# Optimization experiments

Measured on AMD Instinct MI355X. Metric: run time of the kernel, lower is better.

## Reference

```python
import jax, jax.numpy as jnp
import numpy as np
from jax import lax

B, L, E = 16, 100, 128
NQ, NC, DL = 1000, 100, 100
NODE, PATH, MAXC = 5000, 5000, 128


def setup_inputs() -> dict:
    key = jax.random.key(0)
    ks = jax.random.split(key, 40)
    rn = lambda k, *s: jax.random.normal(k, s, jnp.float32) * 0.02
    inp = {}
    inp['code'] = jax.random.randint(ks[0], (B, L, NQ * 2 + MAXC * 3), 0, NODE, jnp.int32)
    inp['q'] = jax.random.randint(ks[1], (B, L), 0, NQ, jnp.int32)
    inp['c'] = jax.random.randint(ks[2], (B, L), 0, NC, jnp.int32)
    inp['sd'] = jax.random.randint(ks[3], (B, L), 0, DL, jnp.int32)
    inp['qd'] = jax.random.randint(ks[4], (B, L), 0, DL, jnp.int32)
    inp['a'] = jax.random.randint(ks[5], (B, L), 0, NQ * 2, jnp.int32)
    inp['qshft'] = jax.random.randint(ks[6], (B, L), 0, NQ, jnp.int32)
    inp['cshft'] = jax.random.randint(ks[7], (B, L), 0, NC, jnp.int32)
    inp['sdshft'] = jax.random.randint(ks[8], (B, L), 0, DL, jnp.int32)
    inp['qdshft'] = jax.random.randint(ks[9], (B, L), 0, DL, jnp.int32)
    # embedding tables (padding rows zeroed, matching torch padding_idx)
    inp['embed_nodes'] = rn(ks[10], NODE + 2, E)
    inp['embed_paths'] = rn(ks[11], PATH + 2, E)
    inp['q_tab'] = rn(ks[12], NQ + 1, E).at[NQ].set(0.0)
    inp['c_tab'] = rn(ks[13], NC + 1, E).at[NC].set(0.0)
    inp['sd_tab'] = rn(ks[14], DL + 100, E).at[0].set(0.0)
    inp['qd_tab'] = rn(ks[15], DL + 100, E).at[0].set(0.0)
    inp['a_tab'] = rn(ks[16], NQ * 2 + 2, E).at[2].set(0.0)
    inp['knowledge'] = rn(ks[17], 1, E)
    # linear weights stored [in, out] so y = x @ W + b
    inp['Wpt'] = rn(ks[18], 3 * E, 3 * E); inp['bpt'] = rn(ks[19], 3 * E)
    inp['Wat'] = rn(ks[20], 3 * E, 1);     inp['bat'] = rn(ks[21], 1)
    inp['Wqa'] = rn(ks[22], 4 * E, E);     inp['bqa'] = rn(ks[23], E)
    inp['W1'] = rn(ks[24], 4 * E, E);      inp['b1'] = rn(ks[25], E)
    inp['W2'] = rn(ks[26], E, E);          inp['b2'] = rn(ks[27], E)
    inp['W3'] = rn(ks[28], E, E);          inp['b3'] = rn(ks[29], E)
    inp['W4'] = rn(ks[30], 2 * E, E);      inp['b4'] = rn(ks[31], E)
    inp['W5'] = rn(ks[32], 2 * E, E);      inp['b5'] = rn(ks[33], E)
    inp['W6'] = rn(ks[34], 4 * E, E);      inp['b6'] = rn(ks[35], E)
    inp['Wf'] = rn(ks[36], E, 10);         inp['bf'] = rn(ks[37], 10)
    return inp


def reference(code, q, c, sd, qd, a, qshft, cshft, sdshft, qdshft,
              embed_nodes, embed_paths, q_tab, c_tab, sd_tab, qd_tab, a_tab,
              knowledge, Wpt, bpt, Wat, bat, Wqa, bqa, W1, b1, W2, b2, W3, b3,
              W4, b4, W5, b5, W6, b6, Wf, bf):
    Bq, Lq = q.shape
    # ---- code2vec attention over AST paths ----
    c2v = code[:, :, NQ * 2:].reshape(Bq, Lq, MAXC, 3)
    full = jnp.concatenate([embed_nodes[c2v[..., 0]],
                            embed_nodes[c2v[..., 2]],
                            embed_paths[c2v[..., 1]]], axis=-1)  # [B,L,MAXC,3E]
    tr = jnp.tanh(full @ Wpt + bpt)
    ctx = tr @ Wat + bat                      # [B,L,MAXC,1]
    attn = jax.nn.softmax(ctx, axis=1)        # softmax over seq dim (dim=1), as in source
    code_vec = jnp.sum(full * attn, axis=2)   # [B,L,3E]
    # ---- embeddings + input projections ----
    a_e = a_tab[a]
    acode = jnp.concatenate([a_e, code_vec], axis=-1) @ Wqa + bqa   # [B,L,E]
    inp = jnp.concatenate([q_tab[q], c_tab[c], sd_tab[sd], qd_tab[qd]], axis=-1) @ W1 + b1
    sd_e = sd_tab[sd]
    qd_e = qd_tab[qd]
    # ---- sequential SDF/PKA/KSU recurrence ----
    k0 = jnp.tile(knowledge, (Bq, 1))  # [B,E]

    def step(k, ts):
        inp_t, a_t, sd_t, qd_t = ts
        qq = inp_t - k
        sdf = jax.nn.sigmoid(qq @ W2 + b2) * jnp.tanh(qq @ W3 + b3)
        x = jnp.concatenate([sdf, a_t], axis=-1)
        pka = jax.nn.sigmoid(x @ W4 + b4) * jnp.tanh(x @ W5 + b5)
        ins = jnp.concatenate([k, a_t, sd_t, qd_t], axis=-1)
        g = jax.nn.sigmoid(ins @ W6 + b6)
        k_new = g * k + (1.0 - g) * pka
        return k_new, k_new @ Wf + bf

    xs = (inp.transpose(1, 0, 2), acode.transpose(1, 0, 2),
          sd_e.transpose(1, 0, 2), qd_e.transpose(1, 0, 2))
    _, logits = lax.scan(step, k0, xs)        # [L,B,10]
    return jax.nn.sigmoid(logits.transpose(1, 0, 2))  # [B,L,10]
```

## Files before the change

### kernel.cpp

```cpp
#include <hip/hip_runtime.h>
#include <hip/hip_bf16.h>

#define B_   16
#define L_   100
#define E_   128
#define NQ_  1000
#define MAXC_ 128
#define CODE_STRIDE (NQ_*2 + MAXC_*3)
#define CODE_OFF    (NQ_*2)

typedef short bf16x8 __attribute__((ext_vector_type(8)));
typedef float f32x4  __attribute__((ext_vector_type(4)));

__device__ __forceinline__ unsigned short f2b(float f) {
    unsigned u = __float_as_uint(f);
    unsigned r = (u + 0x7fffu + ((u >> 16) & 1u)) >> 16;
    return (unsigned short)r;
}
__device__ __forceinline__ unsigned cvt2(float lo, float hi) {
    unsigned r;
    asm("v_cvt_pk_bf16_f32 %0, %1, %2" : "=v"(r) : "v"(lo), "v"(hi));
    return r;
}
__device__ __forceinline__ float fsig(float x) {
    return __builtin_amdgcn_rcpf(1.0f + __builtin_amdgcn_exp2f(-1.44269504f * x));
}
__device__ __forceinline__ float ftanh(float x) {
    return 1.0f - 2.0f * __builtin_amdgcn_rcpf(1.0f + __builtin_amdgcn_exp2f(2.88539008f * x));
}
__device__ __forceinline__ void ldsbar() {
    asm volatile("s_waitcnt lgkmcnt(0)" ::: "memory");
    __builtin_amdgcn_s_barrier();
}
__device__ __forceinline__ void vmbar() {
    asm volatile("s_waitcnt vmcnt(0) lgkmcnt(0)" ::: "memory");
    __builtin_amdgcn_s_barrier();
}
__device__ __forceinline__ void gll16(const void* g, void* l) {
    __builtin_amdgcn_global_load_lds(
        (const __attribute__((address_space(1))) unsigned int*)g,
        (__attribute__((address_space(3))) unsigned int*)l, 16, 0, 0);
}

__global__ void k_prep(const float* __restrict__ Wpt, const float* __restrict__ en,
                       const float* __restrict__ ep,
                       const float* __restrict__ W2, const float* __restrict__ W3,
                       const float* __restrict__ W4, const float* __restrict__ W5,
                       const float* __restrict__ W6, const float* __restrict__ Wf,
                       const float* __restrict__ Wqa, const float* __restrict__ W1,
                       unsigned short* __restrict__ wptT, unsigned short* __restrict__ enb,
                       unsigned short* __restrict__ epb, unsigned short* __restrict__ bt1,
                       unsigned short* __restrict__ bt2, unsigned short* __restrict__ btf,
                       unsigned short* __restrict__ bW1, unsigned short* __restrict__ bW2,
                       unsigned short* __restrict__ bW6)
{
    int i = blockIdx.x * 256 + threadIdx.x;
    switch (blockIdx.y) {
    case 0: if (i < 384*384) {
                int e = i & 7, G = i >> 3;
                int l15g = G & 15, rest = G >> 4;
                int l4g = rest & 3, rest2 = rest >> 2;
                int ksg = rest2 % 12, tile = rest2 / 12;
                int n = tile*16 + l15g, k = ksg*32 + l4g*8 + e;
                wptT[i] = f2b(Wpt[k*384 + n]);
            } break;
    case 1: if (i < 5002*128) enb[i] = f2b(en[i]); break;
    case 2: if (i < 5002*128) epb[i] = f2b(ep[i]); break;
    case 3: if (i < 384*128) {
                int n = i >> 7, k = i & 127;
                float v = (n < 128) ? W2[k*128 + n] : (n < 256) ? W3[k*128 + (n-128)]
                                                                : W6[k*128 + (n-256)];
                bt1[i] = f2b(v);
            } break;
    case 4: if (i < 256*128) {
                int n = i >> 7, k = i & 127;
                float v = (n < 128) ? W4[k*128 + n] : W5[k*128 + (n-128)];
                bt2[i] = f2b(v);
            } break;
    case 5: if (i < 16*128) {
                int n = i >> 7, k = i & 127;
                btf[i] = f2b(n < 10 ? Wf[k*10 + n] : 0.0f);
            } break;
    case 6: if (i < 256*512) {
                int n = i >> 9, k = i & 511;
                float v = (n < 128) ? Wqa[k*128 + n] : W1[k*128 + (n-128)];
                bW1[i] = f2b(v);
            } break;
    case 7: if (i < 512*128) {
                int n = i >> 7, k = i & 127;
                float v = (n < 128) ? W2[k*128 + n]
                        : (n < 256) ? W3[k*128 + (n-128)]
                        : (n < 384) ? W4[(128 + k)*128 + (n-256)]
                                    : W5[(128 + k)*128 + (n-384)];
                bW2[i] = f2b(v);
            } break;
    case 8: if (i < 128*384) {
                int n = i / 384, k = i % 384;
                bW6[i] = f2b(W6[(128 + k)*128 + n]);
            } break;
    }
}

__global__ __launch_bounds__(256, 3) void k_ctx(const int* __restrict__ code,
    const unsigned short* __restrict__ enb, const unsigned short* __restrict__ epb,
    const unsigned short* __restrict__ wptT, const float* __restrict__ bpt,
    const float* __restrict__ wat, const float* __restrict__ bat,
    float* __restrict__ ctx)
{
    __shared__ __align__(16) unsigned short Bs[2][12288];
    __shared__ float bw[768];
    const int tid = threadIdx.x, wv = tid >> 6, lane = tid & 63;
    const int l15 = lane & 15, l4 = lane >> 4;
    const int rowg0 = blockIdx.x * 128;

    for (int idx = tid; idx < 768; idx += 256)
        bw[idx] = (idx < 384) ? bpt[idx] : wat[idx - 384];

    bf16x8 af[2][12];
    #pragma unroll
    for (int h = 0; h < 2; ++h) {
        int rowg = rowg0 + h * 64 + wv * 16 + l15;
        int m = rowg & 127, bl = rowg >> 7;
        const int* cp = code + (size_t)bl * CODE_STRIDE + CODE_OFF + m * 3;
        int i0 = cp[0], i1 = cp[1], i2 = cp[2];
        #pragma unroll
        for (int ks = 0; ks < 12; ++ks) {
            int seg = ks >> 2;
            int idx = (seg == 0) ? i0 : (seg == 1 ? i2 : i1);
            const unsigned short* tab = (seg == 2) ? epb : enb;
            af[h][ks] = *(const bf16x8*)(tab + (size_t)idx * 128 + (ks & 3) * 32 + l4 * 8);
        }
    }

    {
        const unsigned short* src = wptT;
        #pragma unroll
        for (int i = 0; i < 6; ++i) {
            int jj = wv * 6 + i;
            gll16(src + jj * 512 + lane * 8, &Bs[0][jj * 512]);
        }
    }

    float cr[2][4] = {{0.f,0.f,0.f,0.f},{0.f,0.f,0.f,0.f}};
    const float bat0 = bat[0];

    for (int nc = 0; nc < 12; ++nc) {
        vmbar();
        if (nc < 11) {
            const unsigned short* src = wptT + (size_t)(nc + 1) * 12288;
            #pragma unroll
            for (int i = 0; i < 6; ++i) {
                int jj = wv * 6 + i;
                gll16(src + jj * 512 + lane * 8, &Bs[(nc + 1) & 1][jj * 512]);
            }
        }
        const char* bb0 = (const char*)&Bs[nc & 1][0] + l15 * 16;
        const char* bb1 = bb0 + 12288;
        f32x4 acc00 = {0.f,0.f,0.f,0.f}, acc01 = {0.f,0.f,0.f,0.f};
        f32x4 acc10 = {0.f,0.f,0.f,0.f}, acc11 = {0.f,0.f,0.f,0.f};
        #pragma unroll
        for (int ks = 0; ks < 12; ++ks) {
            int go = (ks * 4 + l4) * 256;
            bf16x8 b0 = *(const bf16x8*)(bb0 + go);
            bf16x8 b1 = *(const bf16x8*)(bb1 + go);
            acc00 = __builtin_amdgcn_mfma_f32_16x16x32_bf16(af[0][ks], b0, acc00, 0, 0, 0);
            acc01 = __builtin_amdgcn_mfma_f32_16x16x32_bf16(af[0][ks], b1, acc01, 0, 0, 0);
            acc10 = __builtin_amdgcn_mfma_f32_16x16x32_bf16(af[1][ks], b0, acc10, 0, 0, 0);
            acc11 = __builtin_amdgcn_mfma_f32_16x16x32_bf16(af[1][ks], b1, acc11, 0, 0, 0);
        }
        int ng0 = nc * 32 + l15, ng1 = ng0 + 16;
        float bv0 = bw[ng0], wa0 = bw[384 + ng0];
        float bv1 = bw[ng1], wa1 = bw[384 + ng1];
        #pragma unroll
        for (int r = 0; r < 4; ++r) {
            cr[0][r] += ftanh(acc00[r] + bv0) * wa0 + ftanh(acc01[r] + bv1) * wa1;
            cr[1][r] += ftanh(acc10[r] + bv0) * wa0 + ftanh(acc11[r] + bv1) * wa1;
        }
    }

    #pragma unroll
    for (int h = 0; h < 2; ++h)
        #pragma unroll
        for (int r = 0; r < 4; ++r) {
            float v = cr[h][r];
            v += __shfl_xor(v, 1); v += __shfl_xor(v, 2);
            v += __shfl_xor(v, 4); v += __shfl_xor(v, 8);
            cr[h][r] = v;
        }
    if (l15 == 0) {
        #pragma unroll
        for (int h = 0; h < 2; ++h) {
            int rbase = rowg0 + h * 64 + wv * 16 + l4 * 4;
            #pragma unroll
            for (int r = 0; r < 4; ++r) ctx[rbase + r] = cr[h][r] + bat0;
        }
    }
}

__global__ void k_softmax(const float* __restrict__ ctx, float* __restrict__ attn)
{
    int t = blockIdx.x * 256 + threadIdx.x;
    if (t >= B_ * MAXC_) return;
    int b = t >> 7, m = t & 127;
    const float* p = ctx + (size_t)b * L_ * MAXC_ + m;
    float mx = -1e30f;
    for (int l = 0; l < L_; ++l) mx = fmaxf(mx, p[l * MAXC_]);
    float s = 0.f;
    for (int l = 0; l < L_; ++l) s += __expf(p[l * MAXC_] - mx);
    float inv = 1.0f / s;
    float* o = attn + (size_t)b * L_ * MAXC_ + m;
    for (int l = 0; l < L_; ++l) o[l * MAXC_] = __expf(p[l * MAXC_] - mx) * inv;
}

__global__ __launch_bounds__(192) void k_codevec(const int* __restrict__ code,
    const float* __restrict__ attn, const unsigned short* __restrict__ enb,
    const unsigned short* __restrict__ epb, float* __restrict__ cv)
{
    int bl = blockIdx.x;
    int t = threadIdx.x;
    int seg = t >> 6, tc = t & 63;
    const int* cp = code + (size_t)bl * CODE_STRIDE + CODE_OFF;
    const float* ap = attn + (size_t)bl * MAXC_;
    const unsigned short* tab = (seg == 2) ? epb : enb;
    const int sidx = (seg == 0) ? 0 : (seg == 1) ? 2 : 1;
    float ax = 0.f, ay = 0.f;
    #pragma unroll 8
    for (int m = 0; m < MAXC_; ++m) {
        float w = ap[m];
        int idx = cp[m * 3 + sidx];
        unsigned u = *((const unsigned*)(tab + (size_t)idx * 128) + tc);
        ax += w * __uint_as_float(u << 16);
        ay += w * __uint_as_float(u & 0xffff0000u);
    }
    float2 o; o.x = ax; o.y = ay;
    *(float2*)(cv + (size_t)bl * 384 + seg * 128 + tc * 2) = o;
}

__global__ __launch_bounds__(256) void k_fuse(
    const int* __restrict__ a, const int* __restrict__ q, const int* __restrict__ c,
    const int* __restrict__ sd, const int* __restrict__ qd,
    const float* __restrict__ a_tab, const float* __restrict__ q_tab,
    const float* __restrict__ c_tab, const float* __restrict__ sd_tab,
    const float* __restrict__ qd_tab, const float* __restrict__ cv,
    const unsigned short* __restrict__ bW1, const unsigned short* __restrict__ bW2,
    const unsigned short* __restrict__ bW6,
    const float* __restrict__ bqa, const float* __restrict__ b1,
    const float* __restrict__ b2, const float* __restrict__ b3,
    const float* __restrict__ b4, const float* __restrict__ b5,
    const float* __restrict__ b6,
    float4* __restrict__ preQ, float* __restrict__ pre6)
{
    __shared__ __align__(16) unsigned short X[16 * 1024];
    __shared__ __align__(16) unsigned short Y[16 * 256];
    const int tid = threadIdx.x, wv = tid >> 6, lane = tid & 63;
    const int l15 = lane & 15, l4 = lane >> 4;
    const int row0 = blockIdx.x * 16;

    #pragma unroll
    for (int it = 0; it < 16; ++it) {
        int idx = tid + it * 256;
        int r = idx >> 8, col = (idx & 255) * 4;
        int row = row0 + r;
        const float* src;
        if (col < 128)       src = a_tab + (size_t)a[row] * 128 + col;
        else if (col < 512)  src = cv + (size_t)row * 384 + (col - 128);
        else if (col < 640)  src = q_tab + (size_t)q[row] * 128 + (col - 512);
        else if (col < 768)  src = c_tab + (size_t)c[row] * 128 + (col - 640);
        else if (col < 896)  src = sd_tab + (size_t)sd[row] * 128 + (col - 768);
        else                 src = qd_tab + (size_t)qd[row] * 128 + (col - 896);
        float4 v = *(const float4*)src;
        unsigned u0 = cvt2(v.x, v.y), u1 = cvt2(v.z, v.w);
        int byte = r * 2048 + ((((col >> 3)) ^ (r & 7)) << 4) + ((col & 4) << 1);
        *(unsigned*)((char*)X + byte) = u0;
        *(unsigned*)((char*)X + byte + 4) = u1;
    }
    ldsbar();

    {
        bf16x8 ak[16];
        int kbase = (wv < 2) ? 0 : 512;
        #pragma unroll
        for (int ks = 0; ks < 16; ++ks) {
            int col = kbase + ks * 32 + l4 * 8;
            ak[ks] = *(const bf16x8*)((const char*)X + l15 * 2048 + (((col >> 3) ^ (l15 & 7)) << 4));
        }
        int nbase = wv * 64;
        f32x4 acc[4] = {{0,0,0,0},{0,0,0,0},{0,0,0,0},{0,0,0,0}};
        #pragma unroll
        for (int i = 0; i < 4; ++i) {
            const unsigned short* bp = bW1 + (size_t)(nbase + i * 16 + l15) * 512 + l4 * 8;
            #pragma unroll
            for (int ks = 0; ks < 16; ++ks) {
                bf16x8 bfr = *(const bf16x8*)(bp + ks * 32);
                acc[i] = __builtin_amdgcn_mfma_f32_16x16x32_bf16(ak[ks], bfr, acc[i], 0, 0, 0);
            }
        }
        #pragma unroll
        for (int i = 0; i < 4; ++i) {
            int cc = nbase + i * 16 + l15;
            float bias = (cc < 128) ? bqa[cc] : b1[cc - 128];
            #pragma unroll
            for (int rr = 0; rr < 4; ++rr) {
                int row = l4 * 4 + rr;
                int byte = row * 512 + (((cc >> 3) ^ (row & 7)) << 4) + (cc & 7) * 2;
                *(unsigned short*)((char*)Y + byte) = f2b(acc[i][rr] + bias);
            }
        }
    }
    ldsbar();

    bf16x8 zi[4], za[4], zs[4], zq[4];
    #pragma unroll
    for (int ks = 0; ks < 4; ++ks) {
        int ci = 128 + ks * 32 + l4 * 8;
        zi[ks] = *(const bf16x8*)((const char*)Y + l15 * 512 + (((ci >> 3) ^ (l15 & 7)) << 4));
        int ca = ks * 32 + l4 * 8;
        za[ks] = *(const bf16x8*)((const char*)Y + l15 * 512 + (((ca >> 3) ^ (l15 & 7)) << 4));
        int cs = 768 + ks * 32 + l4 * 8;
        zs[ks] = *(const bf16x8*)((const char*)X + l15 * 2048 + (((cs >> 3) ^ (l15 & 7)) << 4));
        int cq = 896 + ks * 32 + l4 * 8;
        zq[ks] = *(const bf16x8*)((const char*)X + l15 * 2048 + (((cq >> 3) ^ (l15 & 7)) << 4));
    }
    f32x4 A2[2] = {{0,0,0,0},{0,0,0,0}}, A3[2] = {{0,0,0,0},{0,0,0,0}};
    f32x4 A4[2] = {{0,0,0,0},{0,0,0,0}}, A5[2] = {{0,0,0,0},{0,0,0,0}};
    f32x4 A6[2] = {{0,0,0,0},{0,0,0,0}};
    #pragma unroll
    for (int tt = 0; tt < 2; ++tt) {
        int n = wv * 32 + tt * 16 + l15;
        const unsigned short* p2 = bW2 + (size_t)(      n) * 128 + l4 * 8;
        const unsigned short* p3 = bW2 + (size_t)(128 + n) * 128 + l4 * 8;
        const unsigned short* p4 = bW2 + (size_t)(256 + n) * 128 + l4 * 8;
        const unsigned short* p5 = bW2 + (size_t)(384 + n) * 128 + l4 * 8;
        const unsigned short* p6 = bW6 + (size_t)n * 384 + l4 * 8;
        #pragma unroll
        for (int ks = 0; ks < 4; ++ks) {
            A2[tt] = __builtin_amdgcn_mfma_f32_16x16x32_bf16(zi[ks], *(const bf16x8*)(p2 + ks*32), A2[tt], 0, 0, 0);
            A3[tt] = __builtin_amdgcn_mfma_f32_16x16x32_bf16(zi[ks], *(const bf16x8*)(p3 + ks*32), A3[tt], 0, 0, 0);
            A4[tt] = __builtin_amdgcn_mfma_f32_16x16x32_bf16(za[ks], *(const bf16x8*)(p4 + ks*32), A4[tt], 0, 0, 0);
            A5[tt] = __builtin_amdgcn_mfma_f32_16x16x32_bf16(za[ks], *(const bf16x8*)(p5 + ks*32), A5[tt], 0, 0, 0);
            A6[tt] = __builtin_amdgcn_mfma_f32_16x16x32_bf16(za[ks], *(const bf16x8*)(p6 + ks*32), A6[tt], 0, 0, 0);
        }
        #pragma unroll
        for (int ks = 0; ks < 4; ++ks)
            A6[tt] = __builtin_amdgcn_mfma_f32_16x16x32_bf16(zs[ks], *(const bf16x8*)(p6 + 256 + ks*32), A6[tt], 0, 0, 0);
        #pragma unroll
        for (int ks = 0; ks < 4; ++ks)
            A6[tt] = __builtin_amdgcn_mfma_f32_16x16x32_bf16(zq[ks], *(const bf16x8*)(p6 + 512 + ks*32), A6[tt], 0, 0, 0);
    }
    #pragma unroll
    for (int tt = 0; tt < 2; ++tt) {
        int n = wv * 32 + tt * 16 + l15;
        float c2 = b2[n], c3 = b3[n], c4 = b4[n], c5 = b5[n], c6 = b6[n];
        #pragma unroll
        for (int rr = 0; rr < 4; ++rr) {
            size_t row = (size_t)(row0 + l4 * 4 + rr);
            float4 o;
            o.x = A2[tt][rr] + c2; o.y = A3[tt][rr] + c3;
            o.z = A4[tt][rr] + c4; o.w = A5[tt][rr] + c5;
            preQ[row * 128 + n] = o;
            pre6[row * 128 + n] = A6[tt][rr] + c6;
        }
    }
}

__global__ __launch_bounds__(512) void k_recur(
    const unsigned short* __restrict__ bt1, const unsigned short* __restrict__ bt2,
    const float* __restrict__ knowledge, const float4* __restrict__ preQ,
    const float* __restrict__ pre6, unsigned short* __restrict__ khist)
{
    __shared__ __align__(16) unsigned short k_lds[16 * 128];
    __shared__ __align__(16) unsigned short s_lds[16 * 128];
    const int tid = threadIdx.x, wv = tid >> 6, lane = tid & 63;
    const int l15 = lane & 15, l4 = lane >> 4;
    const int j = wv * 16 + l15;

    bf16x8 w2f[4], w3f[4], w6f[4], w4f[4], w5f[4];
    #pragma unroll
    for (int ks = 0; ks < 4; ++ks) {
        w2f[ks] = *(const bf16x8*)(bt1 + (size_t)(      j) * 128 + ks * 32 + l4 * 8);
        w3f[ks] = *(const bf16x8*)(bt1 + (size_t)(128 + j) * 128 + ks * 32 + l4 * 8);
        w6f[ks] = *(const bf16x8*)(bt1 + (size_t)(256 + j) * 128 + ks * 32 + l4 * 8);
        w4f[ks] = *(const bf16x8*)(bt2 + (size_t)(      j) * 128 + ks * 32 + l4 * 8);
        w5f[ks] = *(const bf16x8*)(bt2 + (size_t)(128 + j) * 128 + ks * 32 + l4 * 8);
    }

    float kreg[4], gR[4];
    {
        float k0 = knowledge[j];
        unsigned short kb = f2b(k0);
        #pragma unroll
        for (int r = 0; r < 4; ++r) {
            kreg[r] = k0;
            int b = l4 * 4 + r;
            k_lds[b * 128 + (((j >> 3) ^ b) << 3) + (j & 7)] = kb;
        }
    }
    ldsbar();

    float4 pv[4]; float p6[4];
    #pragma unroll
    for (int r = 0; r < 4; ++r) {
        int b = l4 * 4 + r;
        size_t ix = (size_t)(b * L_) * 128 + j;
        pv[r] = preQ[ix]; p6[r] = pre6[ix];
    }

    for (int t = 0; t < L_; ++t) {
        float4 pvN[4]; float p6N[4];
        #pragma unroll
        for (int r = 0; r < 4; ++r) {
            int b = l4 * 4 + r;
            size_t ix = (size_t)(b * L_ + t + 1) * 128 + j;
            pvN[r] = preQ[ix]; p6N[r] = pre6[ix];
        }

        bf16x8 ak[4];
        {
            const unsigned short* kb = k_lds + l15 * 128;
            #pragma unroll
            for (int ks = 0; ks < 4; ++ks)
                ak[ks] = *(const bf16x8*)(kb + (((ks * 4 + l4) ^ l15) << 3));
        }
        f32x4 a2 = {0,0,0,0}, a3 = {0,0,0,0}, a6 = {0,0,0,0};
        #pragma unroll
        for (int ks = 0; ks < 4; ++ks) {
            a2 = __builtin_amdgcn_mfma_f32_16x16x32_bf16(ak[ks], w2f[ks], a2, 0, 0, 0);
            a3 = __builtin_amdgcn_mfma_f32_16x16x32_bf16(ak[ks], w3f[ks], a3, 0, 0, 0);
            a6 = __builtin_amdgcn_mfma_f32_16x16x32_bf16(ak[ks], w6f[ks], a6, 0, 0, 0);
        }
        #pragma unroll
        for (int r = 0; r < 4; ++r) {
            int b = l4 * 4 + r;
            float sdf = fsig(pv[r].x - a2[r]) * ftanh(pv[r].y - a3[r]);
            gR[r] = fsig(a6[r] + p6[r]);
            s_lds[b * 128 + (((j >> 3) ^ b) << 3) + (j & 7)] = f2b(sdf);
        }
        ldsbar();
        bf16x8 as[4];
        {
            const unsigned short* sb = s_lds + l15 * 128;
            #pragma unroll
            for (int ks = 0; ks < 4; ++ks)
                as[ks] = *(const bf16x8*)(sb + (((ks * 4 + l4) ^ l15) << 3));
        }
        f32x4 a4 = {0,0,0,0}, a5 = {0,0,0,0};
        #pragma unroll
        for (int ks = 0; ks < 4; ++ks) {
            a4 = __builtin_amdgcn_mfma_f32_16x16x32_bf16(as[ks], w4f[ks], a4, 0, 0, 0);
            a5 = __builtin_amdgcn_mfma_f32_16x16x32_bf16(as[ks], w5f[ks], a5, 0, 0, 0);
        }
        #pragma unroll
        for (int r = 0; r < 4; ++r) {
            int b = l4 * 4 + r;
            float pka = fsig(a4[r] + pv[r].z) * ftanh(a5[r] + pv[r].w);
            float kn = gR[r] * kreg[r] + (1.0f - gR[r]) * pka;
            kreg[r] = kn;
            unsigned short kb2 = f2b(kn);
            k_lds[b * 128 + (((j >> 3) ^ b) << 3) + (j & 7)] = kb2;
            khist[(size_t)(b * L_ + t) * 128 + j] = kb2;
        }
        #pragma unroll
        for (int r = 0; r < 4; ++r) { pv[r] = pvN[r]; p6[r] = p6N[r]; }
        ldsbar();
    }
}

__global__ __launch_bounds__(256) void k_logits(const unsigned short* __restrict__ khist,
    const unsigned short* __restrict__ btf, const float* __restrict__ bfv,
    float* __restrict__ out)
{
    int wv = threadIdx.x >> 6, lane = threadIdx.x & 63;
    int l15 = lane & 15, l4 = lane >> 4;
    int R0 = (blockIdx.x * 4 + wv) * 16;
    bf16x8 wbf[4], akr[4];
    #pragma unroll
    for (int ks = 0; ks < 4; ++ks)
        wbf[ks] = *(const bf16x8*)(btf + (size_t)l15 * 128 + ks * 32 + l4 * 8);
    const unsigned short* kb = khist + (size_t)(R0 + l15) * 128;
    #pragma unroll
    for (int ks = 0; ks < 4; ++ks)
        akr[ks] = *(const bf16x8*)(kb + ks * 32 + l4 * 8);
    f32x4 af = {0.f, 0.f, 0.f, 0.f};
    #pragma unroll
    for (int ks = 0; ks < 4; ++ks)
        af = __builtin_amdgcn_mfma_f32_16x16x32_bf16(akr[ks], wbf[ks], af, 0, 0, 0);
    if (l15 < 10) {
        float bb = bfv[l15];
        #pragma unroll
        for (int r = 0; r < 4; ++r)
            out[(size_t)(R0 + l4 * 4 + r) * 10 + l15] = fsig(af[r] + bb);
    }
}

extern "C" void kernel_launch(void* const* d_in, const int* in_sizes, int n_in,
                              void* d_out, int out_size, void* d_ws, size_t ws_size,
                              hipStream_t stream)
{
    const int*   code  = (const int*)d_in[0];
    const int*   q     = (const int*)d_in[1];
    const int*   c     = (const int*)d_in[2];
    const int*   sd    = (const int*)d_in[3];
    const int*   qd    = (const int*)d_in[4];
    const int*   a     = (const int*)d_in[5];
    const float* en    = (const float*)d_in[10];
    const float* ep    = (const float*)d_in[11];
    const float* q_tab = (const float*)d_in[12];
    const float* c_tab = (const float*)d_in[13];
    const float* sd_tab= (const float*)d_in[14];
    const float* qd_tab= (const float*)d_in[15];
    const float* a_tab = (const float*)d_in[16];
    const float* know  = (const float*)d_in[17];
    const float* Wpt   = (const float*)d_in[18];
    const float* bpt   = (const float*)d_in[19];
    const float* Wat   = (const float*)d_in[20];
    const float* bat   = (const float*)d_in[21];
    const float* Wqa   = (const float*)d_in[22];
    const float* bqa   = (const float*)d_in[23];
    const float* W1    = (const float*)d_in[24];
    const float* b1    = (const float*)d_in[25];
    const float* W2    = (const float*)d_in[26];
    const float* b2    = (const float*)d_in[27];
    const float* W3    = (const float*)d_in[28];
    const float* b3    = (const float*)d_in[29];
    const float* W4    = (const float*)d_in[30];
    const float* b4    = (const float*)d_in[31];
    const float* W5    = (const float*)d_in[32];
    const float* b5    = (const float*)d_in[33];
    const float* W6    = (const float*)d_in[34];
    const float* b6    = (const float*)d_in[35];
    const float* Wf    = (const float*)d_in[36];
    const float* bf_   = (const float*)d_in[37];

    char* ws = (char*)d_ws;
    size_t off = 0;
    auto alloc = [&](size_t n) { size_t r = off; off += (n + 255) & ~(size_t)255; return r; };
    unsigned short* wptT = (unsigned short*)(ws + alloc(384 * 384 * 2));
    unsigned short* enb  = (unsigned short*)(ws + alloc(5002 * 128 * 2));
    unsigned short* epb  = (unsigned short*)(ws + alloc(5002 * 128 * 2));
    unsigned short* bt1  = (unsigned short*)(ws + alloc(384 * 128 * 2));
    unsigned short* bt2  = (unsigned short*)(ws + alloc(256 * 128 * 2));
    unsigned short* btf  = (unsigned short*)(ws + alloc(16 * 128 * 2));
    unsigned short* bW1  = (unsigned short*)(ws + alloc(256 * 512 * 2));
    unsigned short* bW2  = (unsigned short*)(ws + alloc(512 * 128 * 2));
    unsigned short* bW6  = (unsigned short*)(ws + alloc(128 * 384 * 2));
    float* ctx   = (float*)(ws + alloc((size_t)B_ * L_ * MAXC_ * 4));
    float* attn  = (float*)(ws + alloc((size_t)B_ * L_ * MAXC_ * 4));
    float* cv    = (float*)(ws + alloc((size_t)B_ * L_ * 384 * 4));
    float4* preQ = (float4*)(ws + alloc(((size_t)B_ * L_ * 128 + 128) * 16));
    float* pre6  = (float*)(ws + alloc(((size_t)B_ * L_ * 128 + 128) * 4));
    unsigned short* khist = (unsigned short*)(ws + alloc((size_t)B_ * L_ * 128 * 2));
    float* outf  = (float*)d_out;

    k_prep<<<dim3(2501, 9), 256, 0, stream>>>(Wpt, en, ep, W2, W3, W4, W5, W6, Wf,
                                              Wqa, W1,
                                              wptT, enb, epb, bt1, bt2, btf,
                                              bW1, bW2, bW6);
    k_ctx<<<1600, 256, 0, stream>>>(code, enb, epb, wptT, bpt, Wat, bat, ctx);
    k_softmax<<<8, 256, 0, stream>>>(ctx, attn);
    k_codevec<<<1600, 192, 0, stream>>>(code, attn, enb, epb, cv);
    k_fuse<<<100, 256, 0, stream>>>(a, q, c, sd, qd, a_tab, q_tab, c_tab, sd_tab,
                                    qd_tab, cv, bW1, bW2, bW6, bqa, b1,
                                    b2, b3, b4, b5, b6, preQ, pre6);
    k_recur<<<1, 512, 0, stream>>>(bt1, bt2, know, preQ, pre6, khist);
    k_logits<<<25, 256, 0, stream>>>(khist, btf, bf_, outf);
}
```

Measured before the change: 290.3 us.

## Triple-buffer ctx weight tiles and fold softmax normalize into codevec

The ctx GEMM now streams the weight matrix in 24 half-size chunks through a three-deep LDS ring, waiting on only part of vmcnt so two loads stay in flight while one chunk is computed. LDS per block drops, which may allow more resident blocks. The softmax kernel now only computes per-column max and reciprocal sum. The exp-and-normalize step moves into codevec, which drops the full attn write and reread. The cost is more barriers per block and exp work repeated inside codevec.

```diff
diff --git a/kernel.cpp b/kernel.cpp
--- a/kernel.cpp
+++ b/kernel.cpp
@@ -30,10 +30,6 @@
 }
 __device__ __forceinline__ void ldsbar() {
     asm volatile("s_waitcnt lgkmcnt(0)" ::: "memory");
-    __builtin_amdgcn_s_barrier();
-}
-__device__ __forceinline__ void vmbar() {
-    asm volatile("s_waitcnt vmcnt(0) lgkmcnt(0)" ::: "memory");
     __builtin_amdgcn_s_barrier();
 }
 __device__ __forceinline__ void gll16(const void* g, void* l) {
@@ -107,7 +103,7 @@
     const float* __restrict__ wat, const float* __restrict__ bat,
     float* __restrict__ ctx)
 {
-    __shared__ __align__(16) unsigned short Bs[2][12288];
+    __shared__ __align__(16) unsigned short Bs[3][6144];
     __shared__ float bw[768];
     const int tid = threadIdx.x, wv = tid >> 6, lane = tid & 63;
     const int l15 = lane & 15, l4 = lane >> 4;
@@ -132,50 +128,49 @@
         }
     }
 
-    {
-        const unsigned short* src = wptT;
-        #pragma unroll
-        for (int i = 0; i < 6; ++i) {
-            int jj = wv * 6 + i;
-            gll16(src + jj * 512 + lane * 8, &Bs[0][jj * 512]);
+    #pragma unroll
+    for (int c = 0; c < 2; ++c) {
+        const unsigned short* src = wptT + c * 6144;
+        #pragma unroll
+        for (int i = 0; i < 3; ++i) {
+            int jj = wv * 3 + i;
+            gll16(src + jj * 512 + lane * 8, &Bs[c][jj * 512]);
         }
     }
 
     float cr[2][4] = {{0.f,0.f,0.f,0.f},{0.f,0.f,0.f,0.f}};
     const float bat0 = bat[0];
 
-    for (int nc = 0; nc < 12; ++nc) {
-        vmbar();
-        if (nc < 11) {
-            const unsigned short* src = wptT + (size_t)(nc + 1) * 12288;
+    int buf = 0;
+    for (int nc = 0; nc < 24; ++nc) {
+        if (nc < 23) asm volatile("s_waitcnt vmcnt(3) lgkmcnt(0)" ::: "memory");
+        else         asm volatile("s_waitcnt vmcnt(0) lgkmcnt(0)" ::: "memory");
+        __builtin_amdgcn_s_barrier();
+        if (nc < 22) {
+            int nb = buf + 2; if (nb >= 3) nb -= 3;
+            const unsigned short* src = wptT + (size_t)(nc + 2) * 6144;
             #pragma unroll
-            for (int i = 0; i < 6; ++i) {
-                int jj = wv * 6 + i;
-                gll16(src + jj * 512 + lane * 8, &Bs[(nc + 1) & 1][jj * 512]);
+            for (int i = 0; i < 3; ++i) {
+                int jj = wv * 3 + i;
+                gll16(src + jj * 512 + lane * 8, &Bs[nb][jj * 512]);
             }
         }
-        const char* bb0 = (const char*)&Bs[nc & 1][0] + l15 * 16;
-        const char* bb1 = bb0 + 12288;
-        f32x4 acc00 = {0.f,0.f,0.f,0.f}, acc01 = {0.f,0.f,0.f,0.f};
-        f32x4 acc10 = {0.f,0.f,0.f,0.f}, acc11 = {0.f,0.f,0.f,0.f};
+        const char* bb0 = (const char*)&Bs[buf][0] + l15 * 16;
+        f32x4 acc0 = {0.f,0.f,0.f,0.f}, acc1 = {0.f,0.f,0.f,0.f};
         #pragma unroll
         for (int ks = 0; ks < 12; ++ks) {
-            int go = (ks * 4 + l4) * 256;
-            bf16x8 b0 = *(const bf16x8*)(bb0 + go);
-            bf16x8 b1 = *(const bf16x8*)(bb1 + go);
-            acc00 = __builtin_amdgcn_mfma_f32_16x16x32_bf16(af[0][ks], b0, acc00, 0, 0, 0);
-            acc01 = __builtin_amdgcn_mfma_f32_16x16x32_bf16(af[0][ks], b1, acc01, 0, 0, 0);
-            acc10 = __builtin_amdgcn_mfma_f32_16x16x32_bf16(af[1][ks], b0, acc10, 0, 0, 0);
-            acc11 = __builtin_amdgcn_mfma_f32_16x16x32_bf16(af[1][ks], b1, acc11, 0, 0, 0);
-        }
-        int ng0 = nc * 32 + l15, ng1 = ng0 + 16;
-        float bv0 = bw[ng0], wa0 = bw[384 + ng0];
-        float bv1 = bw[ng1], wa1 = bw[384 + ng1];
+            bf16x8 b0 = *(const bf16x8*)(bb0 + (ks * 4 + l4) * 256);
+            acc0 = __builtin_amdgcn_mfma_f32_16x16x32_bf16(af[0][ks], b0, acc0, 0, 0, 0);
+            acc1 = __builtin_amdgcn_mfma_f32_16x16x32_bf16(af[1][ks], b0, acc1, 0, 0, 0);
+        }
+        int ng = nc * 16 + l15;
+        float bv = bw[ng], wa = bw[384 + ng];
         #pragma unroll
         for (int r = 0; r < 4; ++r) {
-            cr[0][r] += ftanh(acc00[r] + bv0) * wa0 + ftanh(acc01[r] + bv1) * wa1;
-            cr[1][r] += ftanh(acc10[r] + bv0) * wa0 + ftanh(acc11[r] + bv1) * wa1;
-        }
+            cr[0][r] += ftanh(acc0[r] + bv) * wa;
+            cr[1][r] += ftanh(acc1[r] + bv) * wa;
+        }
+        ++buf; if (buf >= 3) buf = 0;
     }
 
     #pragma unroll
@@ -197,36 +192,43 @@
     }
 }
 
-__global__ void k_softmax(const float* __restrict__ ctx, float* __restrict__ attn)
-{
-    int t = blockIdx.x * 256 + threadIdx.x;
-    if (t >= B_ * MAXC_) return;
-    int b = t >> 7, m = t & 127;
+__global__ __launch_bounds__(128) void k_smred(const float* __restrict__ ctx,
+    float* __restrict__ mxv, float* __restrict__ inv)
+{
+    int b = blockIdx.x, m = threadIdx.x;
     const float* p = ctx + (size_t)b * L_ * MAXC_ + m;
     float mx = -1e30f;
     for (int l = 0; l < L_; ++l) mx = fmaxf(mx, p[l * MAXC_]);
     float s = 0.f;
-    for (int l = 0; l < L_; ++l) s += __expf(p[l * MAXC_] - mx);
-    float inv = 1.0f / s;
-    float* o = attn + (size_t)b * L_ * MAXC_ + m;
-    for (int l = 0; l < L_; ++l) o[l * MAXC_] = __expf(p[l * MAXC_] - mx) * inv;
+    for (int l = 0; l < L_; ++l)
+        s += __builtin_amdgcn_exp2f((p[l * MAXC_] - mx) * 1.44269504f);
+    mxv[b * MAXC_ + m] = mx;
+    inv[b * MAXC_ + m] = __builtin_amdgcn_rcpf(s);
 }
 
 __global__ __launch_bounds__(192) void k_codevec(const int* __restrict__ code,
-    const float* __restrict__ attn, const unsigned short* __restrict__ enb,
+    const float* __restrict__ ctx, const float* __restrict__ mxv,
+    const float* __restrict__ inv, const unsigned short* __restrict__ enb,
     const unsigned short* __restrict__ epb, float* __restrict__ cv)
 {
+    __shared__ float sm[128];
     int bl = blockIdx.x;
     int t = threadIdx.x;
+    int b = bl / 100;
+    if (t < 128) {
+        float v = ctx[(size_t)bl * MAXC_ + t];
+        sm[t] = __builtin_amdgcn_exp2f((v - mxv[b * MAXC_ + t]) * 1.44269504f)
+                * inv[b * MAXC_ + t];
+    }
+    ldsbar();
     int seg = t >> 6, tc = t & 63;
     const int* cp = code + (size_t)bl * CODE_STRIDE + CODE_OFF;
-    const float* ap = attn + (size_t)bl * MAXC_;
     const unsigned short* tab = (seg == 2) ? epb : enb;
     const int sidx = (seg == 0) ? 0 : (seg == 1) ? 2 : 1;
     float ax = 0.f, ay = 0.f;
     #pragma unroll 8
     for (int m = 0; m < MAXC_; ++m) {
-        float w = ap[m];
+        float w = sm[m];
         int idx = cp[m * 3 + sidx];
         unsigned u = *((const unsigned*)(tab + (size_t)idx * 128) + tc);
         ax += w * __uint_as_float(u << 16);
@@ -544,7 +546,8 @@
     unsigned short* bW2  = (unsigned short*)(ws + alloc(512 * 128 * 2));
     unsigned short* bW6  = (unsigned short*)(ws + alloc(128 * 384 * 2));
     float* ctx   = (float*)(ws + alloc((size_t)B_ * L_ * MAXC_ * 4));
-    float* attn  = (float*)(ws + alloc((size_t)B_ * L_ * MAXC_ * 4));
+    float* mxv   = (float*)(ws + alloc((size_t)B_ * MAXC_ * 4));
+    float* inv   = (float*)(ws + alloc((size_t)B_ * MAXC_ * 4));
     float* cv    = (float*)(ws + alloc((size_t)B_ * L_ * 384 * 4));
     float4* preQ = (float4*)(ws + alloc(((size_t)B_ * L_ * 128 + 128) * 16));
     float* pre6  = (float*)(ws + alloc(((size_t)B_ * L_ * 128 + 128) * 4));
@@ -556,8 +559,8 @@
                                               wptT, enb, epb, bt1, bt2, btf,
                                               bW1, bW2, bW6);
     k_ctx<<<1600, 256, 0, stream>>>(code, enb, epb, wptT, bpt, Wat, bat, ctx);
-    k_softmax<<<8, 256, 0, stream>>>(ctx, attn);
-    k_codevec<<<1600, 192, 0, stream>>>(code, attn, enb, epb, cv);
+    k_smred<<<16, 128, 0, stream>>>(ctx, mxv, inv);
+    k_codevec<<<1600, 192, 0, stream>>>(code, ctx, mxv, inv, enb, epb, cv);
     k_fuse<<<100, 256, 0, stream>>>(a, q, c, sd, qd, a_tab, q_tab, c_tab, sd_tab,
                                     qd_tab, cv, bW1, bW2, bW6, bqa, b1,
                                     b2, b3, b4, b5, b6, preQ, pre6);
```

New measurement: 293.1 us. About the same (+1.0%).
